# Optimization experiments

Hardware: AMD Instinct MI355X
Metric: run time of the kernel (lower is better)

## Reference

```python
import jax, jax.numpy as jnp
import numpy as np

B = 4096
D = 1024
N = 9000000
TEMPERATURE = 0.1
GAMMA = 0.8
ALPHA = 0.5
EPS = 1e-14


def setup_inputs() -> dict:
    key = jax.random.key(0)
    k1, k2, k3, k4, k5 = jax.random.split(key, 5)
    zis = jax.random.normal(k1, (B, D), dtype=jnp.float32)
    zjs = jax.random.normal(k2, (B, D), dtype=jnp.float32)
    s_I = jax.random.uniform(k3, (N,), dtype=jnp.float32)
    s_T = jax.random.uniform(k4, (N,), dtype=jnp.float32)
    b_I = jnp.zeros((N,), dtype=jnp.float32)
    b_T = jnp.zeros((N,), dtype=jnp.float32)
    ids = jax.random.randint(k5, (B,), 0, N, dtype=jnp.int64 if jax.config.jax_enable_x64 else jnp.int32)
    return {"zis": zis, "zjs": zjs, "s_I": s_I, "s_T": s_T, "b_I": b_I, "b_T": b_T, "ids": ids}


def reference(zis, zjs, s_I, s_T, b_I, b_T, ids):
    sg = jax.lax.stop_gradient
    # L2 normalize embeddings (norm=True path)
    zis = zis / jnp.linalg.norm(zis, axis=1, keepdims=True)
    zjs = zjs / jnp.linalg.norm(zjs, axis=1, keepdims=True)
    sim = jnp.einsum('id,jd->ij', zis, zjs)            # [B, B]
    diag = jnp.diagonal(sim)                            # [B]
    image_diffs = sim - diag[:, None]
    text_diffs = sim - diag[None, :]
    # detached, temperature-scaled diffs (torch .clone().detach_())
    idd = sg(image_diffs) / TEMPERATURE
    tdd = sg(text_diffs) / TEMPERATURE
    # online max tracking (per-id running max b)
    old_b_I = b_I[ids]                                  # gather [B]
    new_b_I = jnp.maximum(idd.max(axis=1), old_b_I)
    old_b_T = b_T[ids]
    new_b_T = jnp.maximum(tdd.max(axis=0), old_b_T)
    mask_neg = 1.0 - jnp.eye(B, dtype=sim.dtype)
    exp_image_diffs = jnp.exp(idd - new_b_I[:, None]) * mask_neg
    exp_text_diffs = jnp.exp(tdd - new_b_T[None, :]) * mask_neg
    g_I = exp_image_diffs.sum(axis=1) / (B - 1)         # [B]
    g_T = exp_text_diffs.sum(axis=0) / (B - 1)          # [B]
    # EMA of softmax denominator with rescaling for new max
    s_I_new = (1.0 - GAMMA) * s_I[ids] * jnp.exp(old_b_I - new_b_I) + GAMMA * g_I
    s_T_new = (1.0 - GAMMA) * s_T[ids] * jnp.exp(old_b_T - new_b_T) + GAMMA * g_T
    # state writes (side effects in torch; computed for fidelity)
    b_I = b_I.at[ids].set(new_b_I)
    b_T = b_T.at[ids].set(new_b_T)
    s_I = s_I.at[ids].set(s_I_new)
    s_T = s_T.at[ids].set(s_T_new)
    s_I_c = jnp.maximum(s_I_new, EPS)
    s_T_c = jnp.maximum(s_T_new, EPS)
    weights_image = exp_image_diffs / s_I_c[:, None]    # detached weights
    weights_text = exp_text_diffs / s_T_c[None, :]
    image_loss = (weights_image * image_diffs).sum(axis=1) / (B - 1)
    text_loss = (weights_text * text_diffs).sum(axis=0) / (B - 1)
    total_loss = ALPHA * image_loss.mean() + (1.0 - ALPHA) * text_loss.mean()
    return total_loss
```

## Files before the change

kernel.cpp:

```cpp
#include <hip/hip_runtime.h>
#include <stdint.h>

#define B_ 4096
#define D_ 1024
#define BM 256
#define BN 128
#define BK 32
#define NT 32
#define TINV 10.0f
#define LOG2E 1.4426950408889634f
#define KE (TINV * LOG2E)
#define INV_BM1 (1.0f / 4095.0f)

typedef __bf16 bf16x8 __attribute__((ext_vector_type(8)));
typedef float f32x4 __attribute__((ext_vector_type(4)));

__device__ __forceinline__ unsigned short f2bf(float x) {
  uint32_t b = __float_as_uint(x);
  b += 0x7FFF + ((b >> 16) & 1);
  return (unsigned short)(b >> 16);
}
__device__ __forceinline__ float bf2f(unsigned short u) {
  return __uint_as_float(((uint32_t)u) << 16);
}

__device__ __forceinline__ void gload16(const void* g, void* l) {
  __builtin_amdgcn_global_load_lds(
      (const __attribute__((address_space(1))) uint32_t*)g,
      (__attribute__((address_space(3))) uint32_t*)l, 16, 0, 0);
}

__global__ __launch_bounds__(256) void k_normalize(const float* __restrict__ zis,
                                                   const float* __restrict__ zjs,
                                                   unsigned short* __restrict__ Abf,
                                                   unsigned short* __restrict__ Bbf) {
  int r = blockIdx.x;
  const float* src;
  unsigned short* dst;
  if (r < B_) { src = zis + (size_t)r * D_; dst = Abf + (size_t)r * D_; }
  else        { src = zjs + (size_t)(r - B_) * D_; dst = Bbf + (size_t)(r - B_) * D_; }
  int t = threadIdx.x;
  float4 v = reinterpret_cast<const float4*>(src)[t];
  float ss = v.x*v.x + v.y*v.y + v.z*v.z + v.w*v.w;
  #pragma unroll
  for (int o = 32; o >= 1; o >>= 1) ss += __shfl_down(ss, o);
  __shared__ float red[4];
  if ((t & 63) == 0) red[t >> 6] = ss;
  __syncthreads();
  float sc = rsqrtf(red[0] + red[1] + red[2] + red[3]);
  ushort4 o4;
  o4.x = f2bf(v.x * sc); o4.y = f2bf(v.y * sc);
  o4.z = f2bf(v.z * sc); o4.w = f2bf(v.w * sc);
  reinterpret_cast<ushort4*>(dst)[t] = o4;
}

__global__ __launch_bounds__(256, 2) void k_gemm(const unsigned short* __restrict__ A,
                                                 const unsigned short* __restrict__ B,
                                                 unsigned short* __restrict__ C,
                                                 float* __restrict__ diagp) {
  __shared__ unsigned short lds[3][12288];
  const int tid = threadIdx.x;
  const int wid = tid >> 6;
  const int lane = tid & 63;
  const int wm = wid >> 1;
  const int wn = wid & 1;
  const int bRow = blockIdx.y * BM;
  const int bCol = blockIdx.x * BN;
  const unsigned short* Ag = A + (size_t)bRow * D_;
  const unsigned short* Bg = B + (size_t)bCol * D_;

  const int lrow = lane >> 2;
  const int scb  = (((lane & 3) ^ ((lane >> 3) & 3))) * 8;
  const size_t soA0 = (size_t)((wid * 4 + 0) * 16 + lrow) * D_ + scb;
  const size_t soA1 = (size_t)((wid * 4 + 1) * 16 + lrow) * D_ + scb;
  const size_t soA2 = (size_t)((wid * 4 + 2) * 16 + lrow) * D_ + scb;
  const size_t soA3 = (size_t)((wid * 4 + 3) * 16 + lrow) * D_ + scb;
  const size_t soB0 = (size_t)((wid * 2 + 0) * 16 + lrow) * D_ + scb;
  const size_t soB1 = (size_t)((wid * 2 + 1) * 16 + lrow) * D_ + scb;

  const int fr = lane & 15;
  const int kq = lane >> 4;
  const int ce = ((kq ^ ((fr >> 1) & 3)) * 8);

  f32x4 acc[8][4] = {};

#define STAGE(T, SL) {                                                        \
    const unsigned short* gA_ = Ag + (size_t)(T) * BK;                        \
    const unsigned short* gB_ = Bg + (size_t)(T) * BK;                        \
    gload16(gA_ + soA0, &lds[SL][(wid * 4 + 0) * 512]);                       \
    gload16(gA_ + soA1, &lds[SL][(wid * 4 + 1) * 512]);                       \
    gload16(gA_ + soA2, &lds[SL][(wid * 4 + 2) * 512]);                       \
    gload16(gA_ + soA3, &lds[SL][(wid * 4 + 3) * 512]);                       \
    gload16(gB_ + soB0, &lds[SL][8192 + (wid * 2 + 0) * 512]);                \
    gload16(gB_ + soB1, &lds[SL][8192 + (wid * 2 + 1) * 512]); }

  STAGE(0, 0); STAGE(1, 1);
  asm volatile("s_waitcnt vmcnt(6)" ::: "memory");
  __builtin_amdgcn_sched_barrier(0);
  __builtin_amdgcn_s_barrier();
  __builtin_amdgcn_sched_barrier(0);

  int sl = 0, sl2 = 2;
  for (int t = 0; t < NT; ++t) {
    const unsigned short* Lb = lds[sl];
    bf16x8 a[8], b[4];
    #pragma unroll
    for (int m = 0; m < 8; ++m)
      a[m] = *reinterpret_cast<const bf16x8*>(&Lb[(wm*128 + m*16 + fr) * 32 + ce]);
    #pragma unroll
    for (int n = 0; n < 4; ++n)
      b[n] = *reinterpret_cast<const bf16x8*>(&Lb[8192 + (wn*64 + n*16 + fr) * 32 + ce]);
    if (t + 2 < NT) STAGE(t + 2, sl2);
    __builtin_amdgcn_s_setprio(1);
    #pragma unroll
    for (int m = 0; m < 8; ++m)
      #pragma unroll
      for (int n = 0; n < 4; ++n)
        acc[m][n] = __builtin_amdgcn_mfma_f32_16x16x32_bf16(a[m], b[n], acc[m][n], 0, 0, 0);
    __builtin_amdgcn_s_setprio(0);
    if (t < NT - 2) {
      asm volatile("s_waitcnt vmcnt(6)" ::: "memory");
    } else if (t == NT - 2) {
      asm volatile("s_waitcnt vmcnt(0)" ::: "memory");
    }
    __builtin_amdgcn_sched_barrier(0);
    if (t < NT - 1) {
      __builtin_amdgcn_s_barrier();
      __builtin_amdgcn_sched_barrier(0);
    }
    sl = (sl == 2) ? 0 : sl + 1;
    sl2 = (sl2 == 2) ? 0 : sl2 + 1;
  }

  const int fr4 = kq * 4;
  #pragma unroll
  for (int m = 0; m < 8; ++m)
    #pragma unroll
    for (int n = 0; n < 4; ++n)
      #pragma unroll
      for (int q = 0; q < 4; ++q) {
        float v = acc[m][n][q];
        int rg = bRow + wm * 128 + m * 16 + fr4 + q;
        int cg = bCol + wn * 64 + n * 16 + fr;
        if (rg == cg) diagp[rg] = v;
        float p = __shfl_xor(v, 1);
        if (!(lane & 1)) {
          uint32_t u = (uint32_t)f2bf(v) | ((uint32_t)f2bf(p) << 16);
          *reinterpret_cast<uint32_t*>(&C[(size_t)rg * B_ + cg]) = u;
        }
      }
#undef STAGE
}

__global__ __launch_bounds__(1024) void k_fused(const unsigned short* __restrict__ sim,
    const float* __restrict__ diag,
    const float* __restrict__ bI, const float* __restrict__ sI,
    const int* __restrict__ ids,
    float* __restrict__ LI, float* __restrict__ cmax_p,
    float* __restrict__ cE_p, float* __restrict__ cE2_p) {
  const int i0 = blockIdx.x * 16;
  const int t = threadIdx.x;
  const int w = t >> 6, lane = t & 63;
  __shared__ float rowPart[16][16][3];

  float cmax[4], cE[4], cE2[4];
  #pragma unroll
  for (int k = 0; k < 4; ++k) { cmax[k] = -3.4e38f; cE[k] = 0.f; cE2[k] = 0.f; }

  for (int r = 0; r < 16; ++r) {
    const unsigned short* sp = sim + (size_t)(i0 + r) * B_ + t * 4;
    uint2 u0 = *reinterpret_cast<const uint2*>(sp);
    float x[4];
    x[0] = __uint_as_float(u0.x << 16); x[1] = __uint_as_float(u0.x & 0xffff0000u);
    x[2] = __uint_as_float(u0.y << 16); x[3] = __uint_as_float(u0.y & 0xffff0000u);
    float rmx = -3.4e38f, rE = 0.f, rE2 = 0.f;
    #pragma unroll
    for (int k = 0; k < 4; ++k) {
      float e = exp2f(x[k] * KE);
      rmx = fmaxf(rmx, x[k]);
      rE += e;
      rE2 = fmaf(e, x[k], rE2);
      cmax[k] = fmaxf(cmax[k], x[k]);
      cE[k] += e;
      cE2[k] = fmaf(e, x[k], cE2[k]);
    }
    #pragma unroll
    for (int o = 32; o >= 1; o >>= 1) {
      rmx = fmaxf(rmx, __shfl_down(rmx, o));
      rE += __shfl_down(rE, o);
      rE2 += __shfl_down(rE2, o);
    }
    if (lane == 0) { rowPart[r][w][0] = rmx; rowPart[r][w][1] = rE; rowPart[r][w][2] = rE2; }
  }
  __syncthreads();
  if (t < 16) {
    int i = i0 + t;
    float mx = -3.4e38f, E = 0.f, E2 = 0.f;
    #pragma unroll
    for (int k = 0; k < 16; ++k) {
      mx = fmaxf(mx, rowPart[t][k][0]);
      E += rowPart[t][k][1];
      E2 += rowPart[t][k][2];
    }
    float dg = diag[i];
    float ed = exp2f(dg * KE);
    int id = ids[i];
    float oldb = bI[id];
    float newb = fmaxf((mx - dg) * TINV, oldb);
    float sc = exp2f(-(dg * TINV + newb) * LOG2E);
    float S1 = (E - ed) * sc;
    float S2 = (E2 - dg * E) * sc;
    float g = S1 * INV_BM1;
    float sn = 0.2f * sI[id] * exp2f((oldb - newb) * LOG2E) + 0.8f * g;
    LI[i] = S2 / fmaxf(sn, 1e-14f) * INV_BM1;
  }
  size_t base = (size_t)blockIdx.x * B_ + t * 4;
  #pragma unroll
  for (int k = 0; k < 4; ++k) {
    cmax_p[base + k] = cmax[k];
    cE_p[base + k]   = cE[k];
    cE2_p[base + k]  = cE2[k];
  }
}

__global__ __launch_bounds__(256) void k_colred(
    const float* __restrict__ diag,
    const float* __restrict__ cmax_p, const float* __restrict__ cE_p,
    const float* __restrict__ cE2_p,
    const float* __restrict__ bT, const float* __restrict__ sT,
    const int* __restrict__ ids, const float* __restrict__ LI,
    float* __restrict__ partial) {
  const int t = threadIdx.x;
  const int cidx = t >> 5;
  const int sub = t & 31;
  const int j = blockIdx.x * 8 + cidx;
  float mx = -3.4e38f, E = 0.f, E2 = 0.f;
  #pragma unroll
  for (int k = 0; k < 8; ++k) {
    size_t o = (size_t)(sub + 32 * k) * B_ + j;
    mx = fmaxf(mx, cmax_p[o]);
    E += cE_p[o];
    E2 += cE2_p[o];
  }
  #pragma unroll
  for (int o = 16; o >= 1; o >>= 1) {
    mx = fmaxf(mx, __shfl_down(mx, o, 32));
    E += __shfl_down(E, o, 32);
    E2 += __shfl_down(E2, o, 32);
  }
  __shared__ float red[8];
  if (sub == 0) {
    float dg = diag[j];
    float ed = exp2f(dg * KE);
    int id = ids[j];
    float oldb = bT[id];
    float newb = fmaxf((mx - dg) * TINV, oldb);
    float sc = exp2f(-(dg * TINV + newb) * LOG2E);
    float S1 = (E - ed) * sc;
    float S2 = (E2 - dg * E) * sc;
    float g = S1 * INV_BM1;
    float sn = 0.2f * sT[id] * exp2f((oldb - newb) * LOG2E) + 0.8f * g;
    float lt = S2 / fmaxf(sn, 1e-14f) * INV_BM1;
    red[cidx] = (0.5f * LI[j] + 0.5f * lt) * (1.0f / (float)B_);
  }
  __syncthreads();
  if (t == 0) {
    float s = 0.f;
    #pragma unroll
    for (int k = 0; k < 8; ++k) s += red[k];
    partial[blockIdx.x] = s;
  }
}

__global__ void k_final2(const float* __restrict__ partial, float* __restrict__ out) {
  int t = threadIdx.x;
  float v = partial[t];
  #pragma unroll
  for (int o = 32; o >= 1; o >>= 1) v += __shfl_down(v, o);
  __shared__ float red[8];
  if ((t & 63) == 0) red[t >> 6] = v;
  __syncthreads();
  if (t == 0) {
    float s = 0.f;
    #pragma unroll
    for (int k = 0; k < 8; ++k) s += red[k];
    out[0] = s;
  }
}

extern "C" void kernel_launch(void* const* d_in, const int* in_sizes, int n_in,
                              void* d_out, int out_size, void* d_ws, size_t ws_size,
                              hipStream_t stream) {
  const float* zis = (const float*)d_in[0];
  const float* zjs = (const float*)d_in[1];
  const float* s_I = (const float*)d_in[2];
  const float* s_T = (const float*)d_in[3];
  const float* b_I = (const float*)d_in[4];
  const float* b_T = (const float*)d_in[5];
  const int*   ids = (const int*)d_in[6];

  char* ws = (char*)d_ws;
  size_t off = 0;
  auto alloc = [&](size_t bytes) -> void* {
    void* p = ws + off;
    off = (off + bytes + 255) & ~(size_t)255;
    return p;
  };
  unsigned short* Abf = (unsigned short*)alloc((size_t)B_ * D_ * 2);
  unsigned short* Bbf = (unsigned short*)alloc((size_t)B_ * D_ * 2);
  unsigned short* sim = (unsigned short*)alloc((size_t)B_ * B_ * 2);
  float* diag   = (float*)alloc(B_ * 4);
  float* cmax_p = (float*)alloc((size_t)256 * B_ * 4);
  float* cE_p   = (float*)alloc((size_t)256 * B_ * 4);
  float* cE2_p  = (float*)alloc((size_t)256 * B_ * 4);
  float* LI     = (float*)alloc(B_ * 4);
  float* partial = (float*)alloc(512 * 4);

  k_normalize<<<2 * B_, 256, 0, stream>>>(zis, zjs, Abf, Bbf);
  k_gemm<<<dim3(B_ / BN, B_ / BM), 256, 0, stream>>>(Abf, Bbf, sim, diag);
  k_fused<<<256, 1024, 0, stream>>>(sim, diag, b_I, s_I, ids, LI, cmax_p, cE_p, cE2_p);
  k_colred<<<512, 256, 0, stream>>>(diag, cmax_p, cE_p, cE2_p, b_T, s_T, ids, LI, partial);
  k_final2<<<1, 512, 0, stream>>>(partial, (float*)d_out);
}
```

Measured before the change: 93.18 us.

## Shrink GEMM M-tile and load A fragments directly from global into registers

Halves the GEMM block tile to 128x128 and stops staging the A operand through LDS. Each wave now loads its A fragments straight from global memory into double-buffered registers one K-step ahead, while B stays in a triple-buffered LDS pipeline. This cuts LDS use and per-thread accumulators so three blocks can fit per CU, and doubles the grid. The cost is that A rows are re-read by both column-waves without sharing, global loads are less coalesced, and each block gets less reuse.

```diff
diff --git a/kernel.cpp b/kernel.cpp
--- a/kernel.cpp
+++ b/kernel.cpp
@@ -3,7 +3,7 @@
 
 #define B_ 4096
 #define D_ 1024
-#define BM 256
+#define BM 128
 #define BN 128
 #define BK 32
 #define NT 32
@@ -19,9 +19,6 @@
   uint32_t b = __float_as_uint(x);
   b += 0x7FFF + ((b >> 16) & 1);
   return (unsigned short)(b >> 16);
-}
-__device__ __forceinline__ float bf2f(unsigned short u) {
-  return __uint_as_float(((uint32_t)u) << 16);
 }
 
 __device__ __forceinline__ void gload16(const void* g, void* l) {
@@ -54,11 +51,11 @@
   reinterpret_cast<ushort4*>(dst)[t] = o4;
 }
 
-__global__ __launch_bounds__(256, 2) void k_gemm(const unsigned short* __restrict__ A,
+__global__ __launch_bounds__(256, 3) void k_gemm(const unsigned short* __restrict__ A,
                                                  const unsigned short* __restrict__ B,
                                                  unsigned short* __restrict__ C,
                                                  float* __restrict__ diagp) {
-  __shared__ unsigned short lds[3][12288];
+  __shared__ unsigned short ldsB[3][4096];
   const int tid = threadIdx.x;
   const int wid = tid >> 6;
   const int lane = tid & 63;
@@ -71,76 +68,82 @@
 
   const int lrow = lane >> 2;
   const int scb  = (((lane & 3) ^ ((lane >> 3) & 3))) * 8;
-  const size_t soA0 = (size_t)((wid * 4 + 0) * 16 + lrow) * D_ + scb;
-  const size_t soA1 = (size_t)((wid * 4 + 1) * 16 + lrow) * D_ + scb;
-  const size_t soA2 = (size_t)((wid * 4 + 2) * 16 + lrow) * D_ + scb;
-  const size_t soA3 = (size_t)((wid * 4 + 3) * 16 + lrow) * D_ + scb;
-  const size_t soB0 = (size_t)((wid * 2 + 0) * 16 + lrow) * D_ + scb;
-  const size_t soB1 = (size_t)((wid * 2 + 1) * 16 + lrow) * D_ + scb;
+  const size_t soB0 = (size_t)((wid * 32 + lrow)) * D_ + scb;
+  const size_t soB1 = (size_t)((wid * 32 + 16 + lrow)) * D_ + scb;
 
   const int fr = lane & 15;
   const int kq = lane >> 4;
   const int ce = ((kq ^ ((fr >> 1) & 3)) * 8);
 
-  f32x4 acc[8][4] = {};
-
-#define STAGE(T, SL) {                                                        \
-    const unsigned short* gA_ = Ag + (size_t)(T) * BK;                        \
+  const unsigned short* Aw = Ag + (size_t)(wm * 64 + fr) * D_ + kq * 8;
+
+  f32x4 acc[4][4] = {};
+
+#define STAGE_B(T, SL) {                                                      \
     const unsigned short* gB_ = Bg + (size_t)(T) * BK;                        \
-    gload16(gA_ + soA0, &lds[SL][(wid * 4 + 0) * 512]);                       \
-    gload16(gA_ + soA1, &lds[SL][(wid * 4 + 1) * 512]);                       \
-    gload16(gA_ + soA2, &lds[SL][(wid * 4 + 2) * 512]);                       \
-    gload16(gA_ + soA3, &lds[SL][(wid * 4 + 3) * 512]);                       \
-    gload16(gB_ + soB0, &lds[SL][8192 + (wid * 2 + 0) * 512]);                \
-    gload16(gB_ + soB1, &lds[SL][8192 + (wid * 2 + 1) * 512]); }
-
-  STAGE(0, 0); STAGE(1, 1);
-  asm volatile("s_waitcnt vmcnt(6)" ::: "memory");
+    gload16(gB_ + soB0, &ldsB[SL][(wid * 2 + 0) * 512]);                      \
+    gload16(gB_ + soB1, &ldsB[SL][(wid * 2 + 1) * 512]); }
+
+#define LOAD_A(T, SET) {                                                      \
+    const unsigned short* ap_ = Aw + (size_t)(T) * BK;                        \
+    SET[0] = *reinterpret_cast<const bf16x8*>(ap_);                           \
+    SET[1] = *reinterpret_cast<const bf16x8*>(ap_ + 16 * D_);                 \
+    SET[2] = *reinterpret_cast<const bf16x8*>(ap_ + 32 * D_);                 \
+    SET[3] = *reinterpret_cast<const bf16x8*>(ap_ + 48 * D_); }
+
+#define TILE_BODY(T, AUSE, ALOAD)                                             \
+  {                                                                           \
+    if ((T) + 1 < NT) LOAD_A((T) + 1, ALOAD);                                 \
+    bf16x8 b[4];                                                              \
+    const unsigned short* Lb_ = ldsB[sl];                                     \
+    _Pragma("unroll") for (int n = 0; n < 4; ++n)                             \
+      b[n] = *reinterpret_cast<const bf16x8*>(                                \
+          &Lb_[(wn * 64 + n * 16 + fr) * 32 + ce]);                           \
+    if ((T) + 2 < NT) STAGE_B((T) + 2, sl2);                                  \
+    __builtin_amdgcn_s_setprio(1);                                            \
+    _Pragma("unroll") for (int m = 0; m < 4; ++m)                             \
+      _Pragma("unroll") for (int n = 0; n < 4; ++n)                           \
+        acc[m][n] = __builtin_amdgcn_mfma_f32_16x16x32_bf16(                  \
+            AUSE[m], b[n], acc[m][n], 0, 0, 0);                               \
+    __builtin_amdgcn_s_setprio(0);                                            \
+    if ((T) < NT - 2) {                                                       \
+      asm volatile("s_waitcnt vmcnt(2)" ::: "memory");                        \
+    } else if ((T) == NT - 2) {                                               \
+      asm volatile("s_waitcnt vmcnt(0)" ::: "memory");                        \
+    }                                                                         \
+    __builtin_amdgcn_sched_barrier(0);                                        \
+    if ((T) < NT - 1) {                                                       \
+      __builtin_amdgcn_s_barrier();                                           \
+      __builtin_amdgcn_sched_barrier(0);                                      \
+    }                                                                         \
+    sl = (sl == 2) ? 0 : sl + 1;                                              \
+    sl2 = (sl2 == 2) ? 0 : sl2 + 1;                                           \
+  }
+
+  bf16x8 aA[4], aB[4];
+  STAGE_B(0, 0);
+  LOAD_A(0, aA);
+  STAGE_B(1, 1);
+  asm volatile("s_waitcnt vmcnt(2)" ::: "memory");
   __builtin_amdgcn_sched_barrier(0);
   __builtin_amdgcn_s_barrier();
   __builtin_amdgcn_sched_barrier(0);
 
   int sl = 0, sl2 = 2;
-  for (int t = 0; t < NT; ++t) {
-    const unsigned short* Lb = lds[sl];
-    bf16x8 a[8], b[4];
-    #pragma unroll
-    for (int m = 0; m < 8; ++m)
-      a[m] = *reinterpret_cast<const bf16x8*>(&Lb[(wm*128 + m*16 + fr) * 32 + ce]);
-    #pragma unroll
-    for (int n = 0; n < 4; ++n)
-      b[n] = *reinterpret_cast<const bf16x8*>(&Lb[8192 + (wn*64 + n*16 + fr) * 32 + ce]);
-    if (t + 2 < NT) STAGE(t + 2, sl2);
-    __builtin_amdgcn_s_setprio(1);
-    #pragma unroll
-    for (int m = 0; m < 8; ++m)
-      #pragma unroll
-      for (int n = 0; n < 4; ++n)
-        acc[m][n] = __builtin_amdgcn_mfma_f32_16x16x32_bf16(a[m], b[n], acc[m][n], 0, 0, 0);
-    __builtin_amdgcn_s_setprio(0);
-    if (t < NT - 2) {
-      asm volatile("s_waitcnt vmcnt(6)" ::: "memory");
-    } else if (t == NT - 2) {
-      asm volatile("s_waitcnt vmcnt(0)" ::: "memory");
-    }
-    __builtin_amdgcn_sched_barrier(0);
-    if (t < NT - 1) {
-      __builtin_amdgcn_s_barrier();
-      __builtin_amdgcn_sched_barrier(0);
-    }
-    sl = (sl == 2) ? 0 : sl + 1;
-    sl2 = (sl2 == 2) ? 0 : sl2 + 1;
+  for (int tt = 0; tt < NT; tt += 2) {
+    TILE_BODY(tt, aA, aB);
+    TILE_BODY(tt + 1, aB, aA);
   }
 
   const int fr4 = kq * 4;
   #pragma unroll
-  for (int m = 0; m < 8; ++m)
+  for (int m = 0; m < 4; ++m)
     #pragma unroll
     for (int n = 0; n < 4; ++n)
       #pragma unroll
       for (int q = 0; q < 4; ++q) {
         float v = acc[m][n][q];
-        int rg = bRow + wm * 128 + m * 16 + fr4 + q;
+        int rg = bRow + wm * 64 + m * 16 + fr4 + q;
         int cg = bCol + wn * 64 + n * 16 + fr;
         if (rg == cg) diagp[rg] = v;
         float p = __shfl_xor(v, 1);
@@ -149,7 +152,9 @@
           *reinterpret_cast<uint32_t*>(&C[(size_t)rg * B_ + cg]) = u;
         }
       }
-#undef STAGE
+#undef TILE_BODY
+#undef LOAD_A
+#undef STAGE_B
 }
 
 __global__ __launch_bounds__(1024) void k_fused(const unsigned short* __restrict__ sim,
```

Result: slower. 129.6 us (+39.1%).

## Quantize normalized embeddings to FP8 e4m3 and use FP8 MFMA GEMM

Applied to the files above, without the earlier changes.

Normalization now writes e4m3 FP8 instead of bf16, and the similarity GEMM uses fp8 MFMA instructions with BK doubled to 64, 512 threads per block and a new swizzled LDS layout. This halves operand bytes and uses the higher-throughput FP8 matrix path. The cost is precision: the unit-norm entries are near 1/32, and after dividing by temperature and exponentiating, similarity errors may shift the loss beyond tolerance.

```diff
diff --git a/kernel.cpp b/kernel.cpp
--- a/kernel.cpp
+++ b/kernel.cpp
@@ -5,14 +5,13 @@
 #define D_ 1024
 #define BM 256
 #define BN 128
-#define BK 32
-#define NT 32
+#define BK 64
+#define NT 16
 #define TINV 10.0f
 #define LOG2E 1.4426950408889634f
 #define KE (TINV * LOG2E)
 #define INV_BM1 (1.0f / 4095.0f)
 
-typedef __bf16 bf16x8 __attribute__((ext_vector_type(8)));
 typedef float f32x4 __attribute__((ext_vector_type(4)));
 
 __device__ __forceinline__ unsigned short f2bf(float x) {
@@ -20,8 +19,31 @@
   b += 0x7FFF + ((b >> 16) & 1);
   return (unsigned short)(b >> 16);
 }
-__device__ __forceinline__ float bf2f(unsigned short u) {
-  return __uint_as_float(((uint32_t)u) << 16);
+
+__device__ __forceinline__ uint8_t f2e4m3(float x) {
+  uint32_t u = __float_as_uint(x);
+  uint32_t s = (u >> 24) & 0x80;
+  int e = (int)((u >> 23) & 0xFF) - 127;
+  uint32_t m = u & 0x7FFFFF;
+  if (e >= -6) {
+    uint32_t mant = m >> 20;
+    uint32_t rest = m & 0xFFFFF;
+    uint32_t rnd = (rest > 0x80000u) || (rest == 0x80000u && (mant & 1));
+    mant += rnd;
+    uint32_t exp4 = (uint32_t)(e + 7);
+    if (mant == 8) { mant = 0; exp4++; }
+    return (uint8_t)(s | (exp4 << 3) | mant);
+  } else {
+    uint32_t M = 0x800000u | m;
+    int sh = 20 + (-6 - e);
+    if (sh > 31) return (uint8_t)s;
+    uint32_t mant = M >> sh;
+    uint32_t rest = M & ((1u << sh) - 1);
+    uint32_t half = 1u << (sh - 1);
+    uint32_t rnd = (rest > half) || (rest == half && (mant & 1));
+    mant += rnd;
+    return (uint8_t)(s | mant);
+  }
 }
 
 __device__ __forceinline__ void gload16(const void* g, void* l) {
@@ -32,13 +54,13 @@
 
 __global__ __launch_bounds__(256) void k_normalize(const float* __restrict__ zis,
                                                    const float* __restrict__ zjs,
-                                                   unsigned short* __restrict__ Abf,
-                                                   unsigned short* __restrict__ Bbf) {
+                                                   uint8_t* __restrict__ Aq,
+                                                   uint8_t* __restrict__ Bq) {
   int r = blockIdx.x;
   const float* src;
-  unsigned short* dst;
-  if (r < B_) { src = zis + (size_t)r * D_; dst = Abf + (size_t)r * D_; }
-  else        { src = zjs + (size_t)(r - B_) * D_; dst = Bbf + (size_t)(r - B_) * D_; }
+  uint8_t* dst;
+  if (r < B_) { src = zis + (size_t)r * D_; dst = Aq + (size_t)r * D_; }
+  else        { src = zjs + (size_t)(r - B_) * D_; dst = Bq + (size_t)(r - B_) * D_; }
   int t = threadIdx.x;
   float4 v = reinterpret_cast<const float4*>(src)[t];
   float ss = v.x*v.x + v.y*v.y + v.z*v.z + v.w*v.w;
@@ -48,17 +70,17 @@
   if ((t & 63) == 0) red[t >> 6] = ss;
   __syncthreads();
   float sc = rsqrtf(red[0] + red[1] + red[2] + red[3]);
-  ushort4 o4;
-  o4.x = f2bf(v.x * sc); o4.y = f2bf(v.y * sc);
-  o4.z = f2bf(v.z * sc); o4.w = f2bf(v.w * sc);
-  reinterpret_cast<ushort4*>(dst)[t] = o4;
-}
-
-__global__ __launch_bounds__(256, 2) void k_gemm(const unsigned short* __restrict__ A,
-                                                 const unsigned short* __restrict__ B,
+  uchar4 o4;
+  o4.x = f2e4m3(v.x * sc); o4.y = f2e4m3(v.y * sc);
+  o4.z = f2e4m3(v.z * sc); o4.w = f2e4m3(v.w * sc);
+  reinterpret_cast<uchar4*>(dst)[t] = o4;
+}
+
+__global__ __launch_bounds__(512, 4) void k_gemm(const uint8_t* __restrict__ A,
+                                                 const uint8_t* __restrict__ B,
                                                  unsigned short* __restrict__ C,
                                                  float* __restrict__ diagp) {
-  __shared__ unsigned short lds[3][12288];
+  __shared__ uint8_t lds[3][24576];
   const int tid = threadIdx.x;
   const int wid = tid >> 6;
   const int lane = tid & 63;
@@ -66,60 +88,64 @@
   const int wn = wid & 1;
   const int bRow = blockIdx.y * BM;
   const int bCol = blockIdx.x * BN;
-  const unsigned short* Ag = A + (size_t)bRow * D_;
-  const unsigned short* Bg = B + (size_t)bCol * D_;
+  const uint8_t* Ag = A + (size_t)bRow * D_;
+  const uint8_t* Bg = B + (size_t)bCol * D_;
 
   const int lrow = lane >> 2;
-  const int scb  = (((lane & 3) ^ ((lane >> 3) & 3))) * 8;
-  const size_t soA0 = (size_t)((wid * 4 + 0) * 16 + lrow) * D_ + scb;
-  const size_t soA1 = (size_t)((wid * 4 + 1) * 16 + lrow) * D_ + scb;
-  const size_t soA2 = (size_t)((wid * 4 + 2) * 16 + lrow) * D_ + scb;
-  const size_t soA3 = (size_t)((wid * 4 + 3) * 16 + lrow) * D_ + scb;
-  const size_t soB0 = (size_t)((wid * 2 + 0) * 16 + lrow) * D_ + scb;
-  const size_t soB1 = (size_t)((wid * 2 + 1) * 16 + lrow) * D_ + scb;
+  const int scol = ((lane & 3) * 16) ^ (lane & 48);
+  const size_t soA0 = (size_t)(wid * 32 + lrow) * D_ + scol;
+  const size_t soA1 = (size_t)(wid * 32 + 16 + lrow) * D_ + scol;
+  const size_t soB  = (size_t)(wid * 16 + lrow) * D_ + scol;
 
   const int fr = lane & 15;
   const int kq = lane >> 4;
-  const int ce = ((kq ^ ((fr >> 1) & 3)) * 8);
-
-  f32x4 acc[8][4] = {};
+  const int sx = (fr & 12) << 2;
+
+  f32x4 acc[4][4] = {};
 
 #define STAGE(T, SL) {                                                        \
-    const unsigned short* gA_ = Ag + (size_t)(T) * BK;                        \
-    const unsigned short* gB_ = Bg + (size_t)(T) * BK;                        \
-    gload16(gA_ + soA0, &lds[SL][(wid * 4 + 0) * 512]);                       \
-    gload16(gA_ + soA1, &lds[SL][(wid * 4 + 1) * 512]);                       \
-    gload16(gA_ + soA2, &lds[SL][(wid * 4 + 2) * 512]);                       \
-    gload16(gA_ + soA3, &lds[SL][(wid * 4 + 3) * 512]);                       \
-    gload16(gB_ + soB0, &lds[SL][8192 + (wid * 2 + 0) * 512]);                \
-    gload16(gB_ + soB1, &lds[SL][8192 + (wid * 2 + 1) * 512]); }
+    const uint8_t* gA_ = Ag + (size_t)(T) * BK;                               \
+    const uint8_t* gB_ = Bg + (size_t)(T) * BK;                               \
+    gload16(gA_ + soA0, &lds[SL][(2 * wid + 0) * 1024]);                      \
+    gload16(gA_ + soA1, &lds[SL][(2 * wid + 1) * 1024]);                      \
+    gload16(gB_ + soB,  &lds[SL][16384 + wid * 1024]); }
 
   STAGE(0, 0); STAGE(1, 1);
-  asm volatile("s_waitcnt vmcnt(6)" ::: "memory");
+  asm volatile("s_waitcnt vmcnt(3)" ::: "memory");
   __builtin_amdgcn_sched_barrier(0);
   __builtin_amdgcn_s_barrier();
   __builtin_amdgcn_sched_barrier(0);
 
   int sl = 0, sl2 = 2;
   for (int t = 0; t < NT; ++t) {
-    const unsigned short* Lb = lds[sl];
-    bf16x8 a[8], b[4];
-    #pragma unroll
-    for (int m = 0; m < 8; ++m)
-      a[m] = *reinterpret_cast<const bf16x8*>(&Lb[(wm*128 + m*16 + fr) * 32 + ce]);
-    #pragma unroll
-    for (int n = 0; n < 4; ++n)
-      b[n] = *reinterpret_cast<const bf16x8*>(&Lb[8192 + (wn*64 + n*16 + fr) * 32 + ce]);
+    const uint8_t* Lb = lds[sl];
+    long long a8[4][2], b8[4][2];
+    #pragma unroll
+    for (int m = 0; m < 4; ++m) {
+      const uint8_t* rp = &Lb[(wm * 64 + m * 16 + fr) * 64];
+      a8[m][0] = *reinterpret_cast<const long long*>(&rp[(kq * 8) ^ sx]);
+      a8[m][1] = *reinterpret_cast<const long long*>(&rp[(32 + kq * 8) ^ sx]);
+    }
+    #pragma unroll
+    for (int n = 0; n < 4; ++n) {
+      const uint8_t* rp = &Lb[16384 + (wn * 64 + n * 16 + fr) * 64];
+      b8[n][0] = *reinterpret_cast<const long long*>(&rp[(kq * 8) ^ sx]);
+      b8[n][1] = *reinterpret_cast<const long long*>(&rp[(32 + kq * 8) ^ sx]);
+    }
     if (t + 2 < NT) STAGE(t + 2, sl2);
     __builtin_amdgcn_s_setprio(1);
     #pragma unroll
-    for (int m = 0; m < 8; ++m)
+    for (int m = 0; m < 4; ++m)
       #pragma unroll
-      for (int n = 0; n < 4; ++n)
-        acc[m][n] = __builtin_amdgcn_mfma_f32_16x16x32_bf16(a[m], b[n], acc[m][n], 0, 0, 0);
+      for (int n = 0; n < 4; ++n) {
+        acc[m][n] = __builtin_amdgcn_mfma_f32_16x16x32_fp8_fp8(
+            a8[m][0], b8[n][0], acc[m][n], 0, 0, 0);
+        acc[m][n] = __builtin_amdgcn_mfma_f32_16x16x32_fp8_fp8(
+            a8[m][1], b8[n][1], acc[m][n], 0, 0, 0);
+      }
     __builtin_amdgcn_s_setprio(0);
     if (t < NT - 2) {
-      asm volatile("s_waitcnt vmcnt(6)" ::: "memory");
+      asm volatile("s_waitcnt vmcnt(3)" ::: "memory");
     } else if (t == NT - 2) {
       asm volatile("s_waitcnt vmcnt(0)" ::: "memory");
     }
@@ -134,13 +160,13 @@
 
   const int fr4 = kq * 4;
   #pragma unroll
-  for (int m = 0; m < 8; ++m)
+  for (int m = 0; m < 4; ++m)
     #pragma unroll
     for (int n = 0; n < 4; ++n)
       #pragma unroll
       for (int q = 0; q < 4; ++q) {
         float v = acc[m][n][q];
-        int rg = bRow + wm * 128 + m * 16 + fr4 + q;
+        int rg = bRow + wm * 64 + m * 16 + fr4 + q;
         int cg = bCol + wn * 64 + n * 16 + fr;
         if (rg == cg) diagp[rg] = v;
         float p = __shfl_xor(v, 1);
@@ -306,8 +332,8 @@
     off = (off + bytes + 255) & ~(size_t)255;
     return p;
   };
-  unsigned short* Abf = (unsigned short*)alloc((size_t)B_ * D_ * 2);
-  unsigned short* Bbf = (unsigned short*)alloc((size_t)B_ * D_ * 2);
+  uint8_t* Aq = (uint8_t*)alloc((size_t)B_ * D_);
+  uint8_t* Bq = (uint8_t*)alloc((size_t)B_ * D_);
   unsigned short* sim = (unsigned short*)alloc((size_t)B_ * B_ * 2);
   float* diag   = (float*)alloc(B_ * 4);
   float* cmax_p = (float*)alloc((size_t)256 * B_ * 4);
@@ -316,8 +342,8 @@
   float* LI     = (float*)alloc(B_ * 4);
   float* partial = (float*)alloc(512 * 4);
 
-  k_normalize<<<2 * B_, 256, 0, stream>>>(zis, zjs, Abf, Bbf);
-  k_gemm<<<dim3(B_ / BN, B_ / BM), 256, 0, stream>>>(Abf, Bbf, sim, diag);
+  k_normalize<<<2 * B_, 256, 0, stream>>>(zis, zjs, Aq, Bq);
+  k_gemm<<<dim3(B_ / BN, B_ / BM), 512, 0, stream>>>(Aq, Bq, sim, diag);
   k_fused<<<256, 1024, 0, stream>>>(sim, diag, b_I, s_I, ids, LI, cmax_p, cE_p, cE2_p);
   k_colred<<<512, 256, 0, stream>>>(diag, cmax_p, cE_p, cE2_p, b_T, s_T, ids, LI, partial);
   k_final2<<<1, 512, 0, stream>>>(partial, (float*)d_out);
```

After: 80.31 us (median of 2 runs). 13.8% less time.
